# Kernel optimization log

Hardware: AMD Instinct MI355X
Metric: run time of the kernel (lower is better)

Reference implementation:

```python
import jax, jax.numpy as jnp
import numpy as np

D_MODEL = 1024; D_STATE = 128; D_CONV = 4; EXPAND = 2; D_HEAD = 64; NGROUPS = 1; CHUNK = 256
D_INNER = EXPAND * D_MODEL; D_SSM = D_INNER; NHEADS = D_SSM // D_HEAD
CONV_DIM = D_SSM + 2 * NGROUPS * D_STATE
D_IN_PROJ = 2 * D_INNER + 2 * NGROUPS * D_STATE + NHEADS
EPS = 1e-5


def setup_inputs() -> dict:
    key = jax.random.key(0)
    ks = jax.random.split(key, 8)
    B, L = 2, 2048
    u = jax.random.normal(ks[0], (B, L, D_MODEL), jnp.float32)
    W_in = jax.random.normal(ks[1], (D_IN_PROJ, D_MODEL), jnp.float32) * (D_MODEL ** -0.5)
    conv_w = jax.random.normal(ks[2], (CONV_DIM, D_CONV), jnp.float32) * 0.2
    conv_b = jax.random.normal(ks[3], (CONV_DIM,), jnp.float32) * 0.1
    # dt_bias init as in the torch module: inv-softplus of dt ~ LogUniform(1e-3, 1e-1)
    dt = jnp.exp(jax.random.uniform(ks[4], (NHEADS,)) * (np.log(0.1) - np.log(0.001)) + np.log(0.001))
    dt_bias = dt + jnp.log(-jnp.expm1(-dt))
    A_log = jnp.log(jax.random.uniform(ks[5], (NHEADS,), minval=1.0, maxval=16.0))
    D = jnp.ones((NHEADS,), jnp.float32)
    norm_w = jnp.ones((D_SSM,), jnp.float32)
    W_out = jax.random.normal(ks[6], (D_MODEL, D_INNER), jnp.float32) * (D_INNER ** -0.5)
    return dict(u=u, W_in=W_in, conv_w=conv_w, conv_b=conv_b, dt_bias=dt_bias,
                A_log=A_log, D=D, norm_w=norm_w, W_out=W_out)


def _silu(x):
    return x * jax.nn.sigmoid(x)


def reference(u, W_in, conv_w, conv_b, dt_bias, A_log, D, norm_w, W_out):
    B, L, _ = u.shape
    zxbcdt = u @ W_in.T  # (B,L,d_in_proj), d_mlp == 0
    z, xBC, dt_raw = jnp.split(zxbcdt, [D_SSM, D_SSM + CONV_DIM], axis=-1)

    # causal depthwise conv1d (kernel D_CONV) + silu
    xpad = jnp.pad(xBC, ((0, 0), (D_CONV - 1, 0), (0, 0)))
    xBC = sum(xpad[:, k:k + L, :] * conv_w[:, k] for k in range(D_CONV)) + conv_b
    xBC = _silu(xBC)

    x, Bm, Cm = jnp.split(xBC, [D_SSM, D_SSM + NGROUPS * D_STATE], axis=-1)
    x = x.reshape(B, L, NHEADS, D_HEAD)
    Bm = Bm.reshape(B, L, NGROUPS, D_STATE)
    Cm = Cm.reshape(B, L, NGROUPS, D_STATE)

    A = -jnp.exp(A_log)                     # (H,)
    dt = jax.nn.softplus(dt_raw + dt_bias)  # (B,L,H)

    # chunked SSD scan
    nc = L // CHUNK
    hpg = NHEADS // NGROUPS
    xc = x.reshape(B, nc, CHUNK, NHEADS, D_HEAD)
    Bc = jnp.repeat(Bm.reshape(B, nc, CHUNK, NGROUPS, D_STATE), hpg, axis=3)  # (B,nc,C,H,N)
    Cc = jnp.repeat(Cm.reshape(B, nc, CHUNK, NGROUPS, D_STATE), hpg, axis=3)
    dtc = dt.reshape(B, nc, CHUNK, NHEADS)
    dA = dtc * A                 # (B,nc,C,H), negative
    cum = jnp.cumsum(dA, axis=2)  # (B,nc,C,H)

    # intra-chunk: L[l,s] = exp(cum[l]-cum[s]) for s<=l
    tril = jnp.tril(jnp.ones((CHUNK, CHUNK), bool))
    seg = cum[:, :, :, None, :] - cum[:, :, None, :, :]          # (B,nc,l,s,H)
    Lmat = jnp.exp(jnp.where(tril[None, None, :, :, None], seg, -jnp.inf))
    CB = jnp.einsum('bclhn,bcshn->bclsh', Cc, Bc)
    M = CB * Lmat * dtc[:, :, None, :, :]                        # dt applied at source s
    Y_intra = jnp.einsum('bclsh,bcshp->bclhp', M, xc)

    # per-chunk final states
    decay_states = jnp.exp(cum[:, :, -1:, :] - cum)              # (B,nc,C,H)
    S = jnp.einsum('bclhn,bclh,bclhp->bchpn', Bc, decay_states * dtc, xc)

    # inter-chunk recurrence (scan over chunks)
    chunk_decay = jnp.exp(cum[:, :, -1, :])                      # (B,nc,H)

    def step(carry, inp):
        d, s = inp
        new = carry * d[:, :, None, None] + s
        return new, carry  # emit state entering the chunk

    init = jnp.zeros((B, NHEADS, D_HEAD, D_STATE), u.dtype)
    _, prev = jax.lax.scan(step, init, (jnp.moveaxis(chunk_decay, 1, 0), jnp.moveaxis(S, 1, 0)))
    prev = jnp.moveaxis(prev, 0, 1)                              # (B,nc,H,P,N)

    Y_inter = jnp.einsum('bclhn,bclh,bchpn->bclhp', Cc, jnp.exp(cum), prev)

    y = (Y_intra + Y_inter).reshape(B, L, NHEADS, D_HEAD) + D[None, None, :, None] * x
    y = y.reshape(B, L, D_SSM)

    # gated RMSNorm (norm_before_gate=False): gate first, then normalize
    yg = y * _silu(z)
    var = jnp.mean(yg * yg, axis=-1, keepdims=True)
    y = yg * jax.lax.rsqrt(var + EPS) * norm_w

    return y @ W_out.T
```

## Files before the change

### kernel.cpp

```cpp
#include <hip/hip_runtime.h>
#include <hip/hip_bf16.h>
#include <math.h>
#include <stdint.h>

#define BATCH    2
#define SEQ      2048
#define DMODEL   1024
#define DSSM     2048
#define NHEADS   32
#define DHEAD    64
#define DSTATE   128
#define CONVDIM  2304
#define DINPROJ  4384
#define NPAD     4480
#define CHUNK    256
#define NCHUNK   8
#define ROWS     (BATCH*SEQ)
#define NBC      (BATCH*NCHUNK)
#define EPSF     1e-5f
#define CBASE    (DSSM + DSTATE)
#define DTCOL    (DSSM + CONVDIM)

typedef _Float16 half8 __attribute__((ext_vector_type(8)));
typedef _Float16 half4 __attribute__((ext_vector_type(4)));
typedef float f32x4 __attribute__((ext_vector_type(4)));

static __device__ __forceinline__ void gload_lds16(const void* g, void* l) {
    __builtin_amdgcn_global_load_lds(
        (const __attribute__((address_space(1))) uint32_t*)g,
        (__attribute__((address_space(3))) uint32_t*)l, 16, 0, 0);
}

template<int WM, int WN, bool HOUT>
__global__ __launch_bounds__(256) void gemm_f16(const _Float16* __restrict__ A,
                                                const _Float16* __restrict__ B,
                                                void* __restrict__ Cout,
                                                float* __restrict__ dtraw,
                                                int K, int ldc, int Nc) {
    constexpr int BM = 32 * WM;
    constexpr int BN = 32 * WN;
    __shared__ _Float16 As[BM * 64];
    __shared__ _Float16 Bs[BN * 64];
    const int t  = threadIdx.x;
    const int wv = t >> 6;
    const int ln = t & 63;
    const int wr = wv >> 1, wc = wv & 1;

    int nwg = gridDim.x * gridDim.y;
    int bid0 = blockIdx.y * gridDim.x + blockIdx.x;
    int qq = nwg >> 3;
    int swz = (bid0 & 7) * qq + (bid0 >> 3);
    const int tm = (swz / gridDim.x) * BM;
    const int bn = (swz % gridDim.x) * BN;

    const int kb = ln >> 4;
    const int lr = ln & 15;
    const int srow = ln >> 3;
    const int susw = (ln & 7) ^ srow;

    f32x4 acc[WM][WN];
    #pragma unroll
    for (int i = 0; i < WM; ++i)
        #pragma unroll
        for (int j = 0; j < WN; ++j) { f32x4 z = {0.f, 0.f, 0.f, 0.f}; acc[i][j] = z; }

    for (int k0 = 0; k0 < K; k0 += 64) {
        #pragma unroll
        for (int q = 0; q < BM / 32; ++q) {
            int seg = q * 4 + wv;
            int row = seg * 8 + srow;
            const _Float16* src = A + (size_t)(tm + row) * K + k0 + susw * 8;
            gload_lds16(src, (void*)(As + seg * 512));
        }
        #pragma unroll
        for (int q = 0; q < BN / 32; ++q) {
            int seg = q * 4 + wv;
            int row = seg * 8 + srow;
            const _Float16* src = B + (size_t)(bn + row) * K + k0 + susw * 8;
            gload_lds16(src, (void*)(Bs + seg * 512));
        }
        __syncthreads();

        #pragma unroll
        for (int ks = 0; ks < 2; ++ks) {
            half8 af[WM], bf[WN];
            #pragma unroll
            for (int mi = 0; mi < WM; ++mi) {
                int r = wr * (16 * WM) + mi * 16 + lr;
                af[mi] = *(const half8*)(As + r * 64 + (((ks * 4 + kb) ^ (r & 7)) << 3));
            }
            #pragma unroll
            for (int ni = 0; ni < WN; ++ni) {
                int r = wc * (16 * WN) + ni * 16 + lr;
                bf[ni] = *(const half8*)(Bs + r * 64 + (((ks * 4 + kb) ^ (r & 7)) << 3));
            }
            #pragma unroll
            for (int mi = 0; mi < WM; ++mi)
                #pragma unroll
                for (int ni = 0; ni < WN; ++ni)
                    acc[mi][ni] = __builtin_amdgcn_mfma_f32_16x16x32_f16(af[mi], bf[ni], acc[mi][ni], 0, 0, 0);
        }
        __syncthreads();
    }

    #pragma unroll
    for (int mi = 0; mi < WM; ++mi) {
        #pragma unroll
        for (int ni = 0; ni < WN; ++ni) {
            int col = bn + wc * (16 * WN) + ni * 16 + lr;
            if (col < Nc) {
                int row = tm + wr * (16 * WM) + mi * 16 + (ln >> 4) * 4;
                if (HOUT) {
                    _Float16* C = (_Float16*)Cout;
                    #pragma unroll
                    for (int r = 0; r < 4; ++r)
                        C[(size_t)(row + r) * ldc + col] = (_Float16)acc[mi][ni][r];
                    if (col >= DTCOL) {
                        #pragma unroll
                        for (int r = 0; r < 4; ++r)
                            dtraw[(size_t)(col - DTCOL) * ROWS + row + r] = acc[mi][ni][r];
                    }
                } else {
                    float* C = (float*)Cout;
                    #pragma unroll
                    for (int r = 0; r < 4; ++r)
                        C[(size_t)(row + r) * ldc + col] = acc[mi][ni][r];
                }
            }
        }
    }
}

__global__ __launch_bounds__(256) void cast_f16_kernel(const float* __restrict__ src,
                                                       _Float16* __restrict__ dst, int n8) {
    int i = blockIdx.x * 256 + threadIdx.x;
    if (i >= n8) return;
    float4 a = ((const float4*)src)[2 * i];
    float4 b = ((const float4*)src)[2 * i + 1];
    half8 h;
    h[0] = (_Float16)a.x; h[1] = (_Float16)a.y; h[2] = (_Float16)a.z; h[3] = (_Float16)a.w;
    h[4] = (_Float16)b.x; h[5] = (_Float16)b.y; h[6] = (_Float16)b.z; h[7] = (_Float16)b.w;
    ((half8*)dst)[i] = h;
}

__global__ __launch_bounds__(256) void cast_pad_f16_kernel(const float* __restrict__ src,
                                                           _Float16* __restrict__ dst,
                                                           int srcRows, int cols, int n8) {
    int i = blockIdx.x * 256 + threadIdx.x;
    if (i >= n8) return;
    int row = (i * 8) / cols;
    half8 h;
    if (row < srcRows) {
        float4 a = ((const float4*)src)[2 * i];
        float4 b = ((const float4*)src)[2 * i + 1];
        h[0] = (_Float16)a.x; h[1] = (_Float16)a.y; h[2] = (_Float16)a.z; h[3] = (_Float16)a.w;
        h[4] = (_Float16)b.x; h[5] = (_Float16)b.y; h[6] = (_Float16)b.z; h[7] = (_Float16)b.w;
    } else {
        #pragma unroll
        for (int q = 0; q < 8; ++q) h[q] = (_Float16)0.f;
    }
    ((half8*)dst)[i] = h;
}

__global__ __launch_bounds__(256) void conv_silu_kernel(const _Float16* __restrict__ zx,
                                                        const float* __restrict__ conv_w,
                                                        const float* __restrict__ conv_b,
                                                        _Float16* __restrict__ xbc,
                                                        _Float16* __restrict__ xTg,
                                                        _Float16* __restrict__ BTg) {
    __shared__ float zs[67 * 64];
    __shared__ float os[64 * 65];
    const int bid = blockIdx.x;
    const int cg = bid % 36;
    const int bc = bid / 36;
    const int b = bc >> 3, cloc = bc & 7;
    const int c0 = cg * 64;
    const int t = threadIdx.x;

    const int cc = c0 + (t & 63);
    const float w0 = conv_w[cc * 4 + 0], w1 = conv_w[cc * 4 + 1];
    const float w2 = conv_w[cc * 4 + 2], w3 = conv_w[cc * 4 + 3];
    const float bias = conv_b[cc];

    for (int lt = 0; lt < 4; ++lt) {
        const int lbase = cloc * 256 + lt * 64;
        __syncthreads();
        for (int i = t; i < 67 * 64; i += 256) {
            int r = i >> 6, col = i & 63;
            int lseq = lbase - 3 + r;
            float v = 0.f;
            if (lseq >= 0)
                v = (float)zx[((size_t)(b * SEQ + lseq)) * DINPROJ + DSSM + c0 + col];
            zs[i] = v;
        }
        __syncthreads();
        {
            int c = t & 63;
            int w = t >> 6;
            #pragma unroll
            for (int j = 0; j < 16; ++j) {
                int l = w * 16 + j;
                float acc = bias + zs[(l + 0) * 64 + c] * w0 + zs[(l + 1) * 64 + c] * w1
                                 + zs[(l + 2) * 64 + c] * w2 + zs[(l + 3) * 64 + c] * w3;
                os[l * 65 + c] = acc / (1.f + expf(-acc));
            }
        }
        __syncthreads();
        {
            int l = t >> 2, cs = (t & 3) * 16;
            size_t m = (size_t)(b * SEQ + lbase + l);
            half8 h0, h1;
            #pragma unroll
            for (int i = 0; i < 8; ++i) h0[i] = (_Float16)os[l * 65 + cs + i];
            #pragma unroll
            for (int i = 0; i < 8; ++i) h1[i] = (_Float16)os[l * 65 + cs + 8 + i];
            _Float16* dst = xbc + m * CONVDIM + c0 + cs;
            *(half8*)dst = h0;
            *(half8*)(dst + 8) = h1;
        }
        if (c0 < CBASE) {
            int c = t >> 2, ls = (t & 3) * 16;
            int gc = c0 + c;
            half8 h0, h1;
            #pragma unroll
            for (int i = 0; i < 8; ++i) h0[i] = (_Float16)os[(ls + i) * 65 + c];
            #pragma unroll
            for (int i = 0; i < 8; ++i) h1[i] = (_Float16)os[(ls + 8 + i) * 65 + c];
            _Float16* dst;
            if (gc < DSSM)
                dst = xTg + ((size_t)bc * 2048 + gc) * 256 + lt * 64 + ls;
            else
                dst = BTg + ((size_t)bc * 128 + (gc - DSSM)) * 256 + lt * 64 + ls;
            *(half8*)dst = h0;
            *(half8*)(dst + 8) = h1;
        }
    }
}

__global__ __launch_bounds__(256) void dtcum_kernel(const float* __restrict__ dtraw,
                                                    const float* __restrict__ dt_bias,
                                                    const float* __restrict__ A_log,
                                                    float* __restrict__ dtT,
                                                    float* __restrict__ cumT) {
    __shared__ float sv[256];
    const int bid = blockIdx.x;
    const int h = bid & 31, bc = bid >> 5;
    const int t = threadIdx.x;
    float v = dtraw[(size_t)h * ROWS + bc * 256 + t] + dt_bias[h];
    float d = (v > 20.f) ? v : log1pf(expf(v));
    float A = -expf(A_log[h]);
    dtT[(size_t)bid * 256 + t] = d;
    sv[t] = d * A;
    #pragma unroll
    for (int off = 1; off < 256; off <<= 1) {
        __syncthreads();
        float add = (t >= off) ? sv[t - off] : 0.f;
        __syncthreads();
        sv[t] += add;
    }
    __syncthreads();
    cumT[(size_t)bid * 256 + t] = sv[t];
}

__global__ __launch_bounds__(256) void chunk_state_mfma(const _Float16* __restrict__ xTg,
                                                        const _Float16* __restrict__ BTg,
                                                        const float* __restrict__ dtT,
                                                        const float* __restrict__ cumT,
                                                        float* __restrict__ S) {
    int bid = blockIdx.x;
    int bc = bid >> 5;
    __shared__ _Float16 cxs[64 * 64];
    __shared__ _Float16 bts[128 * 64];
    __shared__ float coefL[256];
    const int t = threadIdx.x, w = t >> 6, ln = t & 63;
    const int lr = ln & 15, lg = ln >> 4;

    {
        float cl = cumT[(size_t)bid * 256 + 255];
        coefL[t] = expf(cl - cumT[(size_t)bid * 256 + t]) * dtT[(size_t)bid * 256 + t];
    }

    f32x4 sacc[4][2];
    #pragma unroll
    for (int pi = 0; pi < 4; ++pi)
        #pragma unroll
        for (int ni = 0; ni < 2; ++ni) { f32x4 z = {0.f,0.f,0.f,0.f}; sacc[pi][ni] = z; }

    const _Float16* xTh = xTg + (size_t)bid * 64 * 256;

    for (int kt = 0; kt < 4; ++kt) {
        __syncthreads();
        {
            int p = t >> 2, l0 = (t & 3) * 16;
            const _Float16* src = xTh + (size_t)p * 256 + kt * 64;
            #pragma unroll
            for (int q = 0; q < 2; ++q) {
                int c = l0 + q * 8;
                half8 hv = *(const half8*)(src + c);
                half8 ov;
                #pragma unroll
                for (int j = 0; j < 8; ++j)
                    ov[j] = (_Float16)((float)hv[j] * coefL[kt * 64 + c + j]);
                *(half8*)(cxs + p * 64 + (c ^ ((p & 7) << 3))) = ov;
            }
        }
        #pragma unroll
        for (int q = 0; q < 4; ++q) {
            int seg = w * 4 + q;
            int r = seg * 8 + (ln >> 3);
            int csw = 8 * ((ln & 7) ^ (r & 7));
            const _Float16* src = BTg + ((size_t)bc * 128 + r) * 256 + kt * 64 + csw;
            gload_lds16(src, (void*)(bts + seg * 512));
        }
        __syncthreads();
        #pragma unroll
        for (int kk = 0; kk < 2; ++kk) {
            int c0 = kk * 32 + lg * 8;
            half8 ax[4], bx[2];
            #pragma unroll
            for (int pi = 0; pi < 4; ++pi) {
                int r = pi * 16 + lr;
                ax[pi] = *(const half8*)(cxs + r * 64 + (c0 ^ ((r & 7) << 3)));
            }
            #pragma unroll
            for (int ni = 0; ni < 2; ++ni) {
                int r = w * 32 + ni * 16 + lr;
                bx[ni] = *(const half8*)(bts + r * 64 + (c0 ^ ((r & 7) << 3)));
            }
            #pragma unroll
            for (int pi = 0; pi < 4; ++pi)
                #pragma unroll
                for (int ni = 0; ni < 2; ++ni)
                    sacc[pi][ni] = __builtin_amdgcn_mfma_f32_16x16x32_f16(ax[pi], bx[ni], sacc[pi][ni], 0, 0, 0);
        }
    }
    float* sb = S + (size_t)bid * (DHEAD * DSTATE);
    #pragma unroll
    for (int pi = 0; pi < 4; ++pi)
        #pragma unroll
        for (int ni = 0; ni < 2; ++ni)
            #pragma unroll
            for (int r = 0; r < 4; ++r) {
                int p = pi * 16 + lg * 4 + r;
                int n = w * 32 + ni * 16 + lr;
                sb[p * 128 + n] = sacc[pi][ni][r];
            }
}

__global__ __launch_bounds__(256) void scan_kernel(const float* __restrict__ cumT,
                                                   float* __restrict__ S) {
    int bid = blockIdx.x;
    int h = bid & 31, b = bid >> 5;
    int t = threadIdx.x;
    float carry[32];
    #pragma unroll
    for (int i = 0; i < 32; ++i) carry[i] = 0.f;
    for (int c = 0; c < NCHUNK; ++c) {
        int bc = b * NCHUNK + c;
        float decay = expf(cumT[((size_t)(bc * 32 + h)) * 256 + 255]);
        size_t base = ((size_t)(bc * NHEADS + h)) * (DHEAD * DSTATE);
        #pragma unroll
        for (int i = 0; i < 32; ++i) {
            size_t idx = base + t + i * 256;
            float s = S[idx];
            float nw = carry[i] * decay + s;
            S[idx] = carry[i];
            carry[i] = nw;
        }
    }
}

__global__ __launch_bounds__(256, 2) void y_mfma(const _Float16* __restrict__ xbc,
                                                 const _Float16* __restrict__ xTg,
                                                 const float* __restrict__ dtT,
                                                 const float* __restrict__ cumT,
                                                 const float* __restrict__ Sprev,
                                                 const float* __restrict__ Dp,
                                                 float* __restrict__ y) {
    int bid = blockIdx.x;
    int h = bid & 31, bc = bid >> 5;
    __shared__ _Float16 Bs2[2][64 * 128];
    __shared__ _Float16 PwF[4 * 64 * 64];
    __shared__ float cumL[256], dtL[256];
    const int t = threadIdx.x, w = t >> 6, ln = t & 63;
    const int lr = ln & 15, lg = ln >> 4;

    {
        cumL[t] = cumT[(size_t)bid * 256 + t];
        dtL[t]  = dtT[(size_t)bid * 256 + t];
    }
    {
        const float* sp = Sprev + (size_t)bid * (DHEAD * DSTATE);
        int r = t >> 2, cb = (t & 3) * 32;
        #pragma unroll
        for (int q = 0; q < 4; ++q) {
            int c = cb + q * 8;
            float4 f0 = *(const float4*)(sp + r * 128 + c);
            float4 f1 = *(const float4*)(sp + r * 128 + c + 4);
            half8 hv;
            hv[0]=(_Float16)f0.x; hv[1]=(_Float16)f0.y; hv[2]=(_Float16)f0.z; hv[3]=(_Float16)f0.w;
            hv[4]=(_Float16)f1.x; hv[5]=(_Float16)f1.y; hv[6]=(_Float16)f1.z; hv[7]=(_Float16)f1.w;
            *(half8*)(PwF + r * 128 + (c ^ ((r & 7) << 3))) = hv;
        }
    }
    {
        #pragma unroll
        for (int q = 0; q < 4; ++q) {
            int seg = w * 4 + q;
            int r = seg * 4 + lg;
            int csw = 8 * (lr ^ (r & 7));
            const _Float16* src = xbc + ((size_t)(bc * 256 + r)) * CONVDIM + DSSM + csw;
            gload_lds16(src, (void*)(Bs2[0] + seg * 512));
        }
    }
    half8 ca[4][4];
    {
        const _Float16* cb = xbc + ((size_t)(bc * 256 + w * 64)) * CONVDIM + CBASE;
        #pragma unroll
        for (int mi = 0; mi < 4; ++mi)
            #pragma unroll
            for (int kk = 0; kk < 4; ++kk)
                ca[mi][kk] = *(const half8*)(cb + (size_t)(mi * 16 + lr) * CONVDIM + kk * 32 + lg * 8);
    }
    __syncthreads();

    f32x4 yacc[4][4];
    #pragma unroll
    for (int i = 0; i < 4; ++i)
        #pragma unroll
        for (int j = 0; j < 4; ++j) { f32x4 z = {0.f,0.f,0.f,0.f}; yacc[i][j] = z; }

    #pragma unroll
    for (int kk = 0; kk < 4; ++kk) {
        int co = kk * 32 + lg * 8;
        #pragma unroll
        for (int pi = 0; pi < 4; ++pi) {
            int r = pi * 16 + lr;
            half8 pb = *(const half8*)(PwF + r * 128 + (co ^ ((r & 7) << 3)));
            #pragma unroll
            for (int mi = 0; mi < 4; ++mi)
                yacc[mi][pi] = __builtin_amdgcn_mfma_f32_16x16x32_f16(ca[mi][kk], pb, yacc[mi][pi], 0, 0, 0);
        }
    }
    #pragma unroll
    for (int mi = 0; mi < 4; ++mi)
        #pragma unroll
        for (int r = 0; r < 4; ++r) {
            float e = expf(cumL[w * 64 + mi * 16 + lg * 4 + r]);
            #pragma unroll
            for (int pi = 0; pi < 4; ++pi) yacc[mi][pi][r] *= e;
        }
    float c0 = cumL[w * 64];
    float el[4];
    #pragma unroll
    for (int mi = 0; mi < 4; ++mi) el[mi] = expf(cumL[w * 64 + mi * 16 + lr] - c0);
    float Dv = Dp[h];

    __syncthreads();

    _Float16* pwb = PwF + w * 4096;
    for (int st = 0; st < 4; ++st) {
        if (st < 3) {
            #pragma unroll
            for (int q = 0; q < 4; ++q) {
                int seg = w * 4 + q;
                int r = seg * 4 + lg;
                int csw = 8 * (lr ^ (r & 7));
                const _Float16* src = xbc + ((size_t)(bc * 256 + (st + 1) * 64 + r)) * CONVDIM + DSSM + csw;
                gload_lds16(src, (void*)(Bs2[(st + 1) & 1] + seg * 512));
            }
        }
        if (st <= w) {
            const _Float16* bsc = Bs2[st & 1];
            half8 xb[4][2];
            #pragma unroll
            for (int pi = 0; pi < 4; ++pi)
                #pragma unroll
                for (int k2 = 0; k2 < 2; ++k2)
                    xb[pi][k2] = *(const half8*)(xTg + ((size_t)bid * 64 + pi * 16 + lr) * 256
                                                 + st * 64 + k2 * 32 + lg * 8);
            #pragma unroll
            for (int si = 0; si < 4; ++si) {
                f32x4 ps[4];
                #pragma unroll
                for (int mi = 0; mi < 4; ++mi) { f32x4 z = {0.f,0.f,0.f,0.f}; ps[mi] = z; }
                int r = si * 16 + lr;
                #pragma unroll
                for (int kk = 0; kk < 4; ++kk) {
                    int co = kk * 32 + lg * 8;
                    half8 bb = *(const half8*)(bsc + r * 128 + (co ^ ((r & 7) << 3)));
                    #pragma unroll
                    for (int mi = 0; mi < 4; ++mi)
                        ps[mi] = __builtin_amdgcn_mfma_f32_16x16x32_f16(bb, ca[mi][kk], ps[mi], 0, 0, 0);
                }
                if (st < w) {
                    float fs[4];
                    #pragma unroll
                    for (int rr = 0; rr < 4; ++rr) {
                        int sg = st * 64 + si * 16 + lg * 4 + rr;
                        fs[rr] = expf(c0 - cumL[sg]) * dtL[sg];
                    }
                    #pragma unroll
                    for (int mi = 0; mi < 4; ++mi) {
                        half4 hv;
                        #pragma unroll
                        for (int rr = 0; rr < 4; ++rr)
                            hv[rr] = (_Float16)(ps[mi][rr] * el[mi] * fs[rr]);
                        *(half4*)(pwb + (mi * 16 + lr) * 64 + ((si * 16 + lg * 4) ^ (8 * (lr & 7)))) = hv;
                    }
                } else {
                    #pragma unroll
                    for (int mi = 0; mi < 4; ++mi) {
                        int lloc = mi * 16 + lr;
                        float cl = cumL[w * 64 + lloc];
                        half4 hv;
                        #pragma unroll
                        for (int rr = 0; rr < 4; ++rr) {
                            int sl = si * 16 + lg * 4 + rr;
                            float v = 0.f;
                            if (sl <= lloc) {
                                int sg = w * 64 + sl;
                                v = ps[mi][rr] * expf(cl - cumL[sg]) * dtL[sg];
                                if (sl == lloc) v += Dv;
                            }
                            hv[rr] = (_Float16)v;
                        }
                        *(half4*)(pwb + (mi * 16 + lr) * 64 + ((si * 16 + lg * 4) ^ (8 * (lr & 7)))) = hv;
                    }
                }
            }
            #pragma unroll
            for (int k2 = 0; k2 < 2; ++k2) {
                int co = k2 * 32 + lg * 8;
                half8 pa[4];
                #pragma unroll
                for (int mi = 0; mi < 4; ++mi) {
                    int r = mi * 16 + lr;
                    pa[mi] = *(const half8*)(pwb + r * 64 + (co ^ (8 * (lr & 7))));
                }
                #pragma unroll
                for (int pi = 0; pi < 4; ++pi)
                    #pragma unroll
                    for (int mi = 0; mi < 4; ++mi)
                        yacc[mi][pi] = __builtin_amdgcn_mfma_f32_16x16x32_f16(pa[mi], xb[pi][k2], yacc[mi][pi], 0, 0, 0);
            }
        }
        __syncthreads();
    }

    #pragma unroll
    for (int mi = 0; mi < 4; ++mi) {
        #pragma unroll
        for (int r = 0; r < 4; ++r) {
            int l = w * 64 + mi * 16 + lg * 4 + r;
            size_t row = (size_t)bc * 256 + l;
            #pragma unroll
            for (int pi = 0; pi < 4; ++pi)
                y[row * DSSM + h * 64 + pi * 16 + lr] = yacc[mi][pi][r];
        }
    }
}

__global__ __launch_bounds__(256) void norm_kernel(const float* __restrict__ y,
                                                   const _Float16* __restrict__ zx,
                                                   const float* __restrict__ norm_w,
                                                   _Float16* __restrict__ outh) {
    int m = blockIdx.x;
    int t = threadIdx.x;
    const float* yrow = y + (size_t)m * DSSM;
    const _Float16* zrow = zx + (size_t)m * DINPROJ;
    float yg[8];
    float ss = 0.f;
    half8 zv = *(const half8*)(zrow + t * 8);
    float4 yv0 = *(const float4*)(yrow + t * 8);
    float4 yv1 = *(const float4*)(yrow + t * 8 + 4);
    float yvals[8] = {yv0.x, yv0.y, yv0.z, yv0.w, yv1.x, yv1.y, yv1.z, yv1.w};
    #pragma unroll
    for (int i = 0; i < 8; ++i) {
        float z = (float)zv[i];
        float sz = z / (1.f + expf(-z));
        float g = yvals[i] * sz;
        yg[i] = g;
        ss += g * g;
    }
    #pragma unroll
    for (int off = 32; off > 0; off >>= 1) ss += __shfl_xor(ss, off, 64);
    __shared__ float red[4];
    if ((t & 63) == 0) red[t >> 6] = ss;
    __syncthreads();
    float tot = red[0] + red[1] + red[2] + red[3];
    float inv = rsqrtf(tot / (float)DSSM + EPSF);
    half8 h;
    #pragma unroll
    for (int q = 0; q < 8; ++q)
        h[q] = (_Float16)(yg[q] * inv * norm_w[t*8 + q]);
    *(half8*)(outh + (size_t)m * DSSM + t * 8) = h;
}

extern "C" void kernel_launch(void* const* d_in, const int* in_sizes, int n_in,
                              void* d_out, int out_size, void* d_ws, size_t ws_size,
                              hipStream_t stream) {
    (void)in_sizes; (void)n_in; (void)out_size; (void)ws_size;
    const float* u       = (const float*)d_in[0];
    const float* W_in    = (const float*)d_in[1];
    const float* conv_w  = (const float*)d_in[2];
    const float* conv_b  = (const float*)d_in[3];
    const float* dt_bias = (const float*)d_in[4];
    const float* A_log   = (const float*)d_in[5];
    const float* Dp      = (const float*)d_in[6];
    const float* norm_w  = (const float*)d_in[7];
    const float* W_out   = (const float*)d_in[8];
    float* out = (float*)d_out;

    float* dtraw = (float*)d_ws;
    float* dtb   = dtraw + (size_t)ROWS * NHEADS;
    float* cum   = dtb   + (size_t)ROWS * NHEADS;
    float* Sbuf  = cum   + (size_t)ROWS * NHEADS;
    float* yb    = Sbuf  + (size_t)NBC * NHEADS * DHEAD * DSTATE;
    _Float16* zxh   = (_Float16*)(yb + (size_t)ROWS * DSSM);
    _Float16* xbc_h = zxh   + (size_t)ROWS * DINPROJ;
    _Float16* xTg   = xbc_h + (size_t)ROWS * CONVDIM;
    _Float16* BTg   = xTg   + (size_t)NBC * NHEADS * 64 * 256;
    _Float16* uh    = BTg   + (size_t)NBC * 128 * 256;
    _Float16* Wih   = uh    + (size_t)ROWS * DMODEL;
    _Float16* Wouth = Wih   + (size_t)NPAD * DMODEL;
    _Float16* ybh   = Wouth + (size_t)DMODEL * DSSM;

    cast_f16_kernel<<<(ROWS * DMODEL / 8 + 255) / 256, 256, 0, stream>>>(u, uh, ROWS * DMODEL / 8);
    cast_pad_f16_kernel<<<(NPAD * DMODEL / 8 + 255) / 256, 256, 0, stream>>>(
        W_in, Wih, DINPROJ, DMODEL, NPAD * DMODEL / 8);
    cast_f16_kernel<<<(DMODEL * DSSM / 8 + 255) / 256, 256, 0, stream>>>(W_out, Wouth, DMODEL * DSSM / 8);

    gemm_f16<4, 4, true><<<dim3(NPAD / 128, ROWS / 128), 256, 0, stream>>>(
        uh, Wih, (void*)zxh, dtraw, DMODEL, DINPROJ, DINPROJ);
    conv_silu_kernel<<<NBC * 36, 256, 0, stream>>>(
        zxh, conv_w, conv_b, xbc_h, xTg, BTg);
    dtcum_kernel<<<NBC * NHEADS, 256, 0, stream>>>(dtraw, dt_bias, A_log, dtb, cum);
    chunk_state_mfma<<<NBC * NHEADS, 256, 0, stream>>>(xTg, BTg, dtb, cum, Sbuf);
    scan_kernel<<<BATCH * NHEADS, 256, 0, stream>>>(cum, Sbuf);
    y_mfma<<<NBC * NHEADS, 256, 0, stream>>>(xbc_h, xTg, dtb, cum, Sbuf, Dp, yb);
    norm_kernel<<<ROWS, 256, 0, stream>>>(yb, zxh, norm_w, ybh);
    gemm_f16<4, 2, false><<<dim3(DMODEL / 64, ROWS / 128), 256, 0, stream>>>(
        ybh, Wouth, (void*)out, nullptr, DSSM, DMODEL, DMODEL);
}
```

Baseline: 300.1 us.

## Double-buffer GEMM LDS tiles, parallelize chunk scan, store y in fp16

The GEMM kernel now double-buffers its LDS tiles, issuing the next K-tile's global-to-LDS loads before computing the current one and raising wave priority during the MFMA section, with one barrier per iteration. The inter-chunk scan is split across 8 blocks per (batch, head), each handling a 1024-element slice of the state, so it launches 512 blocks instead of 64. The y output between the SSD kernel and the norm kernel is stored as fp16 instead of fp32, halving that round trip. Risks are extra LDS use per GEMM block, which may lower occupancy, and a small precision loss from rounding y to fp16 before normalization.

```diff
diff --git a/kernel.cpp b/kernel.cpp
--- a/kernel.cpp
+++ b/kernel.cpp
@@ -39,8 +39,8 @@
                                                 int K, int ldc, int Nc) {
     constexpr int BM = 32 * WM;
     constexpr int BN = 32 * WN;
-    __shared__ _Float16 As[BM * 64];
-    __shared__ _Float16 Bs[BN * 64];
+    __shared__ _Float16 As[2][BM * 64];
+    __shared__ _Float16 Bs[2][BN * 64];
     const int t  = threadIdx.x;
     const int wv = t >> 6;
     const int ln = t & 63;
@@ -64,35 +64,43 @@
         #pragma unroll
         for (int j = 0; j < WN; ++j) { f32x4 z = {0.f, 0.f, 0.f, 0.f}; acc[i][j] = z; }
 
-    for (int k0 = 0; k0 < K; k0 += 64) {
+    auto stage = [&](int buf, int k0) {
         #pragma unroll
         for (int q = 0; q < BM / 32; ++q) {
             int seg = q * 4 + wv;
             int row = seg * 8 + srow;
             const _Float16* src = A + (size_t)(tm + row) * K + k0 + susw * 8;
-            gload_lds16(src, (void*)(As + seg * 512));
+            gload_lds16(src, (void*)(As[buf] + seg * 512));
         }
         #pragma unroll
         for (int q = 0; q < BN / 32; ++q) {
             int seg = q * 4 + wv;
             int row = seg * 8 + srow;
             const _Float16* src = B + (size_t)(bn + row) * K + k0 + susw * 8;
-            gload_lds16(src, (void*)(Bs + seg * 512));
-        }
-        __syncthreads();
-
+            gload_lds16(src, (void*)(Bs[buf] + seg * 512));
+        }
+    };
+
+    stage(0, 0);
+    __syncthreads();
+    int cur = 0;
+
+    for (int k0 = 0; k0 < K; k0 += 64) {
+        if (k0 + 64 < K) stage(cur ^ 1, k0 + 64);
+
+        __builtin_amdgcn_s_setprio(1);
         #pragma unroll
         for (int ks = 0; ks < 2; ++ks) {
             half8 af[WM], bf[WN];
             #pragma unroll
             for (int mi = 0; mi < WM; ++mi) {
                 int r = wr * (16 * WM) + mi * 16 + lr;
-                af[mi] = *(const half8*)(As + r * 64 + (((ks * 4 + kb) ^ (r & 7)) << 3));
+                af[mi] = *(const half8*)(As[cur] + r * 64 + (((ks * 4 + kb) ^ (r & 7)) << 3));
             }
             #pragma unroll
             for (int ni = 0; ni < WN; ++ni) {
                 int r = wc * (16 * WN) + ni * 16 + lr;
-                bf[ni] = *(const half8*)(Bs + r * 64 + (((ks * 4 + kb) ^ (r & 7)) << 3));
+                bf[ni] = *(const half8*)(Bs[cur] + r * 64 + (((ks * 4 + kb) ^ (r & 7)) << 3));
             }
             #pragma unroll
             for (int mi = 0; mi < WM; ++mi)
@@ -100,7 +108,9 @@
                 for (int ni = 0; ni < WN; ++ni)
                     acc[mi][ni] = __builtin_amdgcn_mfma_f32_16x16x32_f16(af[mi], bf[ni], acc[mi][ni], 0, 0, 0);
         }
-        __syncthreads();
+        __builtin_amdgcn_s_setprio(0);
+        __syncthreads();
+        cur ^= 1;
     }
 
     #pragma unroll
@@ -350,17 +360,19 @@
 __global__ __launch_bounds__(256) void scan_kernel(const float* __restrict__ cumT,
                                                    float* __restrict__ S) {
     int bid = blockIdx.x;
-    int h = bid & 31, b = bid >> 5;
+    int part = bid & 7;
+    int bh = bid >> 3;
+    int h = bh & 31, b = bh >> 5;
     int t = threadIdx.x;
-    float carry[32];
-    #pragma unroll
-    for (int i = 0; i < 32; ++i) carry[i] = 0.f;
+    float carry[4];
+    #pragma unroll
+    for (int i = 0; i < 4; ++i) carry[i] = 0.f;
     for (int c = 0; c < NCHUNK; ++c) {
         int bc = b * NCHUNK + c;
         float decay = expf(cumT[((size_t)(bc * 32 + h)) * 256 + 255]);
-        size_t base = ((size_t)(bc * NHEADS + h)) * (DHEAD * DSTATE);
-        #pragma unroll
-        for (int i = 0; i < 32; ++i) {
+        size_t base = ((size_t)(bc * 32 + h)) * (DHEAD * DSTATE) + part * 1024;
+        #pragma unroll
+        for (int i = 0; i < 4; ++i) {
             size_t idx = base + t + i * 256;
             float s = S[idx];
             float nw = carry[i] * decay + s;
@@ -376,7 +388,7 @@
                                                  const float* __restrict__ cumT,
                                                  const float* __restrict__ Sprev,
                                                  const float* __restrict__ Dp,
-                                                 float* __restrict__ y) {
+                                                 _Float16* __restrict__ y) {
     int bid = blockIdx.x;
     int h = bid & 31, bc = bid >> 5;
     __shared__ _Float16 Bs2[2][64 * 128];
@@ -556,30 +568,28 @@
             size_t row = (size_t)bc * 256 + l;
             #pragma unroll
             for (int pi = 0; pi < 4; ++pi)
-                y[row * DSSM + h * 64 + pi * 16 + lr] = yacc[mi][pi][r];
-        }
-    }
-}
-
-__global__ __launch_bounds__(256) void norm_kernel(const float* __restrict__ y,
+                y[row * DSSM + h * 64 + pi * 16 + lr] = (_Float16)yacc[mi][pi][r];
+        }
+    }
+}
+
+__global__ __launch_bounds__(256) void norm_kernel(const _Float16* __restrict__ y,
                                                    const _Float16* __restrict__ zx,
                                                    const float* __restrict__ norm_w,
                                                    _Float16* __restrict__ outh) {
     int m = blockIdx.x;
     int t = threadIdx.x;
-    const float* yrow = y + (size_t)m * DSSM;
+    const _Float16* yrow = y + (size_t)m * DSSM;
     const _Float16* zrow = zx + (size_t)m * DINPROJ;
     float yg[8];
     float ss = 0.f;
     half8 zv = *(const half8*)(zrow + t * 8);
-    float4 yv0 = *(const float4*)(yrow + t * 8);
-    float4 yv1 = *(const float4*)(yrow + t * 8 + 4);
-    float yvals[8] = {yv0.x, yv0.y, yv0.z, yv0.w, yv1.x, yv1.y, yv1.z, yv1.w};
+    half8 yv = *(const half8*)(yrow + t * 8);
     #pragma unroll
     for (int i = 0; i < 8; ++i) {
         float z = (float)zv[i];
         float sz = z / (1.f + expf(-z));
-        float g = yvals[i] * sz;
+        float g = (float)yv[i] * sz;
         yg[i] = g;
         ss += g * g;
     }
@@ -616,15 +626,15 @@
     float* dtb   = dtraw + (size_t)ROWS * NHEADS;
     float* cum   = dtb   + (size_t)ROWS * NHEADS;
     float* Sbuf  = cum   + (size_t)ROWS * NHEADS;
-    float* yb    = Sbuf  + (size_t)NBC * NHEADS * DHEAD * DSTATE;
-    _Float16* zxh   = (_Float16*)(yb + (size_t)ROWS * DSSM);
+    _Float16* zxh   = (_Float16*)(Sbuf + (size_t)NBC * NHEADS * DHEAD * DSTATE);
     _Float16* xbc_h = zxh   + (size_t)ROWS * DINPROJ;
     _Float16* xTg   = xbc_h + (size_t)ROWS * CONVDIM;
     _Float16* BTg   = xTg   + (size_t)NBC * NHEADS * 64 * 256;
-    _Float16* uh    = BTg   + (size_t)NBC * 128 * 256;
+    _Float16* ybh16 = BTg   + (size_t)NBC * 128 * 256;
+    _Float16* uh    = ybh16 + (size_t)ROWS * DSSM;
     _Float16* Wih   = uh    + (size_t)ROWS * DMODEL;
     _Float16* Wouth = Wih   + (size_t)NPAD * DMODEL;
-    _Float16* ybh   = Wouth + (size_t)DMODEL * DSSM;
+    _Float16* ygh   = Wouth + (size_t)DMODEL * DSSM;
 
     cast_f16_kernel<<<(ROWS * DMODEL / 8 + 255) / 256, 256, 0, stream>>>(u, uh, ROWS * DMODEL / 8);
     cast_pad_f16_kernel<<<(NPAD * DMODEL / 8 + 255) / 256, 256, 0, stream>>>(
@@ -637,9 +647,9 @@
         zxh, conv_w, conv_b, xbc_h, xTg, BTg);
     dtcum_kernel<<<NBC * NHEADS, 256, 0, stream>>>(dtraw, dt_bias, A_log, dtb, cum);
     chunk_state_mfma<<<NBC * NHEADS, 256, 0, stream>>>(xTg, BTg, dtb, cum, Sbuf);
-    scan_kernel<<<BATCH * NHEADS, 256, 0, stream>>>(cum, Sbuf);
-    y_mfma<<<NBC * NHEADS, 256, 0, stream>>>(xbc_h, xTg, dtb, cum, Sbuf, Dp, yb);
-    norm_kernel<<<ROWS, 256, 0, stream>>>(yb, zxh, norm_w, ybh);
+    scan_kernel<<<NBC * NHEADS, 256, 0, stream>>>(cum, Sbuf);
+    y_mfma<<<NBC * NHEADS, 256, 0, stream>>>(xbc_h, xTg, dtb, cum, Sbuf, Dp, ybh16);
+    norm_kernel<<<ROWS, 256, 0, stream>>>(ybh16, zxh, norm_w, ygh);
     gemm_f16<4, 2, false><<<dim3(DMODEL / 64, ROWS / 128), 256, 0, stream>>>(
-        ybh, Wouth, (void*)out, nullptr, DSSM, DMODEL, DMODEL);
-}
+        ygh, Wouth, (void*)out, nullptr, DSSM, DMODEL, DMODEL);
+}
```

Measured after the change: 289.3 us. 1.04x faster.
